# Performance work log

Hardware: AMD Instinct MI355X
Metric: run time of the kernel (lower is better)

The kernel has to match this reference:

```python
import jax, jax.numpy as jnp
import numpy as np

N = 50000          # nodes
E = 400000         # edges
MUL = 32           # multiplicity per irrep
NUM_NEIGHBORS = 8.0
INV_SQRT3 = 1.0 / np.sqrt(3.0)  # w3j(1,1,0) coefficient


def setup_inputs() -> dict:
    key = jax.random.key(0)
    ks = jax.random.split(key, 20)
    inp = {
        # node_input: 32x0e (dim 32) + 32x1o (dim 96) = 128
        "node_input": jax.random.normal(ks[0], (N, 4 * MUL), jnp.float32),
        "node_attr": jnp.ones((N, 1), jnp.float32),           # 1x0e trivial attr
        "edge_src": jax.random.randint(ks[1], (E,), 0, N, jnp.int32),
        "edge_dst": jax.random.randint(ks[2], (E,), 0, N, jnp.int32),
        "edge_attr": jax.random.normal(ks[3], (E, 4), jnp.float32),   # 1x0e + 1x1o
        "edge_scalars": jax.random.normal(ks[4], (E, 16), jnp.float32),
        # FullyConnectedTensorProduct weights (uvw, node_attr has mul 1)
        "w_sc0": jax.random.normal(ks[5], (MUL, MUL), jnp.float32),
        "w_sc1": jax.random.normal(ks[6], (MUL, MUL), jnp.float32),
        "w_lin1_0": jax.random.normal(ks[7], (MUL, MUL), jnp.float32),
        "w_lin1_1": jax.random.normal(ks[8], (MUL, MUL), jnp.float32),
        # radial FC net -> per-edge TP weights (numel = 4*MUL = 128)
        "fc_w1": jax.random.normal(ks[9], (16, 64), jnp.float32),
        "fc_w2": jax.random.normal(ks[10], (64, 4 * MUL), jnp.float32),
        # lin2: irreps_mid (64x0e+64x1o) x attr -> output
        "w_lin2_0": jax.random.normal(ks[11], (2 * MUL, MUL), jnp.float32),
        "w_lin2_1": jax.random.normal(ks[12], (2 * MUL, MUL), jnp.float32),
        # alpha: irreps_mid x attr -> 0e (zero-init in original; small randn for a nontrivial test)
        "w_alpha": 0.1 * jax.random.normal(ks[13], (2 * MUL, 1), jnp.float32),
        # sc_edges: irreps_mid x edge_attr -> edge_attr
        "w_se0a": jax.random.normal(ks[14], (2 * MUL,), jnp.float32),  # mid0e x ea0e -> 0e
        "w_se0b": jax.random.normal(ks[15], (2 * MUL,), jnp.float32),  # mid1o x ea1o -> 0e
        "w_se1a": jax.random.normal(ks[16], (2 * MUL,), jnp.float32),  # mid0e x ea1o -> 1o
        "w_se1b": jax.random.normal(ks[17], (2 * MUL,), jnp.float32),  # mid1o x ea0e -> 1o
    }
    return inp


def reference(node_input, node_attr, edge_src, edge_dst, edge_attr, edge_scalars,
              w_sc0, w_sc1, w_lin1_0, w_lin1_1, fc_w1, fc_w2,
              w_lin2_0, w_lin2_1, w_alpha, w_se0a, w_se0b, w_se1a, w_se1b):
    inv_nn = 1.0 / jnp.sqrt(jnp.asarray(NUM_NEIGHBORS, node_input.dtype))
    n = node_input.shape[0]
    x0 = node_input[:, :MUL]                       # (N, 32)   32x0e
    x1 = node_input[:, MUL:].reshape(n, MUL, 3)    # (N, 32, 3) 32x1o
    a = node_attr                                  # (N, 1)
    s_in = 1.0 / np.sqrt(MUL)                      # FCTP fan-in normalization

    # self-connection: FCTP(input, attr) -> output
    sc0 = (x0 @ w_sc0) * a * s_in
    sc1 = jnp.einsum('num,uw->nwm', x1, w_sc1) * a[:, :, None] * s_in
    node_self = jnp.concatenate([sc0, sc1.reshape(n, 3 * MUL)], axis=1)  # (N, 128)

    # lin1: FCTP(input, attr) -> input irreps
    f0 = (x0 @ w_lin1_0) * a * s_in
    f1 = jnp.einsum('num,uw->nwm', x1, w_lin1_1) * a[:, :, None] * s_in

    # gather source node features per edge
    g0 = f0[edge_src]                              # (E, 32)
    g1 = f1[edge_src]                              # (E, 32, 3)
    ea0 = edge_attr[:, :1]                         # (E, 1)   1x0e
    ea1 = edge_attr[:, 1:]                         # (E, 3)   1x1o

    # radial net -> per-edge TP weights (FullyConnectedNet with sin activation)
    h = jnp.sin(edge_scalars @ fc_w1 * (1.0 / np.sqrt(16.0)))
    w = h @ fc_w2 * (1.0 / np.sqrt(64.0))          # (E, 128)
    wA, wB, wC, wD = jnp.split(w, 4, axis=1)       # each (E, 32)

    # uvu tensor product, 4 instructions
    mA = wA * g0 * ea0                                           # 0e x 0e -> 0e
    mD = wD * jnp.einsum('eum,em->eu', g1, ea1) * INV_SQRT3      # 1o x 1o -> 0e
    mB = (wB * g0)[:, :, None] * ea1[:, None, :]                 # 0e x 1o -> 1o
    mC = (wC[:, :, None] * g1) * ea0[:, :, None]                 # 1o x 0e -> 1o
    mid0 = jnp.concatenate([mA, mD], axis=1)       # (E, 64)  64x0e
    mid1 = jnp.concatenate([mB, mC], axis=1)       # (E, 64, 3) 64x1o

    # scatter-add to destination nodes
    n0 = jax.ops.segment_sum(mid0, edge_dst, num_segments=n) * inv_nn
    n1 = jax.ops.segment_sum(mid1, edge_dst, num_segments=n) * inv_nn

    s_mid = 1.0 / np.sqrt(2 * MUL)
    out0 = (n0 @ w_lin2_0) * a * s_mid
    out1 = jnp.einsum('num,uw->nwm', n1, w_lin2_1) * a[:, :, None] * s_mid
    node_conv = jnp.concatenate([out0, out1.reshape(n, 3 * MUL)], axis=1)

    # alpha gate (sc.output_mask is all ones here, so alpha = 1 - 1 + alpha*1)
    alpha = (n0 @ w_alpha) * a * s_mid             # (N, 1)
    node_conv_out = node_self + alpha * node_conv  # (N, 128)

    # sc_edges: FCTP(mid, edge_attr) -> edge_attr irreps; fan-in = 128 per output
    s_se = 1.0 / np.sqrt(4 * MUL)
    se0 = ((mid0 @ w_se0a) * ea0[:, 0]
           + jnp.einsum('eum,em,u->e', mid1, ea1, w_se0b) * INV_SQRT3) * s_se
    se1 = ((mid0 @ w_se1a)[:, None] * ea1
           + jnp.einsum('eum,u->em', mid1, w_se1b) * ea0) * s_se
    edge_conv_out = edge_attr + jnp.concatenate([se0[:, None], se1], axis=1) * inv_nn

    return node_conv_out, edge_conv_out
```

## Files before the change

### kernel.cpp

```cpp
#include <hip/hip_runtime.h>
#include <math.h>

#define N_NODES 50000
#define E_EDGES 400000
#define NPRE_BLOCKS 6250
#define NHIST_BLOCKS 1563

typedef _Float16 f16x2 __attribute__((ext_vector_type(2)));
typedef _Float16 f16x4 __attribute__((ext_vector_type(4)));
typedef _Float16 f16x8 __attribute__((ext_vector_type(8)));
typedef float    f32x4 __attribute__((ext_vector_type(4)));

static constexpr float S_IN      = 0.17677669529663687f;
static constexpr float S_MID     = 0.125f;
static constexpr float S_SE      = 0.08838834764831843f;
static constexpr float INV_NN    = 0.35355339059327373f;
static constexpr float INV_SQRT3 = 0.5773502691896258f;
static constexpr float FC1_S     = 0.25f;
static constexpr float FC2_S     = 0.125f;

__device__ inline float wave_reduce_dpp(float v) {
    int x;
    x = __builtin_amdgcn_update_dpp(0, __float_as_int(v), 0x111, 0xf, 0xf, true); v += __int_as_float(x);
    x = __builtin_amdgcn_update_dpp(0, __float_as_int(v), 0x112, 0xf, 0xf, true); v += __int_as_float(x);
    x = __builtin_amdgcn_update_dpp(0, __float_as_int(v), 0x114, 0xf, 0xf, true); v += __int_as_float(x);
    x = __builtin_amdgcn_update_dpp(0, __float_as_int(v), 0x118, 0xf, 0xf, true); v += __int_as_float(x);
    x = __builtin_amdgcn_update_dpp(0, __float_as_int(v), 0x142, 0xa, 0xf, true); v += __int_as_float(x);
    x = __builtin_amdgcn_update_dpp(0, __float_as_int(v), 0x143, 0xc, 0xf, true); v += __int_as_float(x);
    return __int_as_float(__builtin_amdgcn_readlane(__float_as_int(v), 63));
}

__global__ __launch_bounds__(256) void pre_hist_kernel(
    const float* __restrict__ node_input, const float* __restrict__ node_attr,
    const float* __restrict__ w_sc0, const float* __restrict__ w_sc1,
    const float* __restrict__ w_lin1_0, const float* __restrict__ w_lin1_1,
    float* __restrict__ out_self, float* __restrict__ ws_f,
    const int* __restrict__ edge_dst, int* __restrict__ counts)
{
    const int t = threadIdx.x;
    if (blockIdx.x >= NPRE_BLOCKS) {
        const int e = (blockIdx.x - NPRE_BLOCKS) * 256 + t;
        if (e < E_EDGES) atomicAdd(&counts[edge_dst[e]], 1);
        return;
    }
    const int n0 = blockIdx.x * 8;
    __shared__ __align__(16) float sx[8 * 128];
    __shared__ float sa[8];
    ((float4*)sx)[t] = ((const float4*)(node_input + (size_t)n0 * 128))[t];
    if (t < 8) sa[t] = node_attr[n0 + t];
    __syncthreads();

    const int half = t >> 7;
    const int idx  = t & 127;
    float wcol[32];
    int m = 0;
    if (idx < 32) {
        const float* __restrict__ W = half ? w_lin1_0 : w_sc0;
        #pragma unroll
        for (int u = 0; u < 32; ++u) wcol[u] = W[u * 32 + idx];
    } else {
        const float* __restrict__ W = half ? w_lin1_1 : w_sc1;
        const int j = idx - 32;
        const int w = j / 3; m = j % 3;
        #pragma unroll
        for (int u = 0; u < 32; ++u) wcol[u] = W[u * 32 + w];
    }
    float* __restrict__ dstp = half ? ws_f : out_self;
    #pragma unroll
    for (int k = 0; k < 8; ++k) {
        const float* x = sx + k * 128;
        float acc = 0.f;
        if (idx < 32) {
            #pragma unroll
            for (int u = 0; u < 32; ++u) acc += x[u] * wcol[u];
        } else {
            #pragma unroll
            for (int u = 0; u < 32; ++u) acc += x[32 + u * 3 + m] * wcol[u];
        }
        dstp[(size_t)(n0 + k) * 128 + idx] = acc * sa[k] * S_IN;
    }
}

__global__ __launch_bounds__(1024) void scan_block_kernel(
    const int* __restrict__ counts, int* __restrict__ cursor, int* __restrict__ bsum)
{
    __shared__ int sd[1024];
    const int t   = threadIdx.x;
    const int idx = blockIdx.x * 1024 + t;
    const int c   = (idx < N_NODES) ? counts[idx] : 0;
    sd[t] = c;
    __syncthreads();
    for (int off = 1; off < 1024; off <<= 1) {
        const int v = (t >= off) ? sd[t - off] : 0;
        __syncthreads();
        sd[t] += v;
        __syncthreads();
    }
    if (idx < N_NODES) cursor[idx] = sd[t] - c;
    if (t == 1023) bsum[blockIdx.x] = sd[1023];
}

__global__ __launch_bounds__(1024) void scan_fixup_kernel(
    int* __restrict__ cursor, const int* __restrict__ bsum)
{
    __shared__ int boff_s;
    const int t = threadIdx.x;
    if (t < 64) {
        int v = (t < (int)blockIdx.x) ? bsum[t] : 0;
        #pragma unroll
        for (int off = 32; off >= 1; off >>= 1) v += __shfl_down(v, off, 64);
        if (t == 0) boff_s = v;
    }
    __syncthreads();
    const int idx = blockIdx.x * 1024 + t;
    if (idx < N_NODES) cursor[idx] += boff_s;
}

__global__ __launch_bounds__(256) void scatter_kernel(
    const int* __restrict__ edge_dst, int* __restrict__ cursor,
    int* __restrict__ sorted_eid)
{
    const int e = blockIdx.x * 256 + threadIdx.x;
    if (e < E_EDGES) {
        const int p = atomicAdd(&cursor[edge_dst[e]], 1);
        sorted_eid[p] = e;
    }
}

__global__ __launch_bounds__(256, 4) void edge_kernel(
    const float* __restrict__ ws_f,
    const int* __restrict__ edge_src, const int* __restrict__ edge_dst,
    const float* __restrict__ edge_attr, const float* __restrict__ edge_scalars,
    const float* __restrict__ fc_w1, const float* __restrict__ fc_w2,
    const float* __restrict__ w_se0a, const float* __restrict__ w_se0b,
    const float* __restrict__ w_se1a, const float* __restrict__ w_se1b,
    const int* __restrict__ sorted_eid,
    float* __restrict__ nacc, float* __restrict__ edge_out)
{
    __shared__ __align__(16) _Float16 sArena[18944];
    __shared__ __align__(16) float sEA[64 * 4];
    __shared__ __align__(16) float sDep[4][36];
    __shared__ int sSRC[64];
    __shared__ int sDST[64];
    __shared__ int sEID[64];

    _Float16* __restrict__ sW2T  = sArena;
    _Float16* __restrict__ sHT   = sArena + 9216;
    _Float16* __restrict__ sES   = sArena + 13824;
    _Float16* __restrict__ sW1T  = sArena + 16384;
    _Float16* __restrict__ sWt   = sArena;
    _Float16* __restrict__ sMidA = sArena + 8704;
    _Float16* __restrict__ sBT   = sArena + 12928;

    const int t    = threadIdx.x;
    const int lane = t & 63;
    const int wv   = t >> 6;
    const int quad = lane >> 4;
    const int mm   = lane & 15;
    const int e0   = blockIdx.x * 64;

    {
        const int k = t >> 4, n4 = (t & 15) * 4;
        float4 v = ((const float4*)fc_w1)[t];
        sW1T[(n4 + 0) * 40 + k] = (_Float16)v.x;
        sW1T[(n4 + 1) * 40 + k] = (_Float16)v.y;
        sW1T[(n4 + 2) * 40 + k] = (_Float16)v.z;
        sW1T[(n4 + 3) * 40 + k] = (_Float16)v.w;
        const f16x4 z4 = {(_Float16)0.f, (_Float16)0.f, (_Float16)0.f, (_Float16)0.f};
        *(f16x4*)&sW1T[(t >> 2) * 40 + 16 + (t & 3) * 4] = z4;
    }
    #pragma unroll
    for (int i = 0; i < 8; ++i) {
        const int u = t + i * 256;
        const int k = u >> 5, c4 = (u & 31) * 4;
        float4 v = ((const float4*)fc_w2)[u];
        sW2T[(c4 + 0) * 72 + k] = (_Float16)v.x;
        sW2T[(c4 + 1) * 72 + k] = (_Float16)v.y;
        sW2T[(c4 + 2) * 72 + k] = (_Float16)v.z;
        sW2T[(c4 + 3) * 72 + k] = (_Float16)v.w;
    }
    {
        const int e = t >> 2, k4 = (t & 3) * 4;
        const int eid = sorted_eid[e0 + e];
        float4 v = ((const float4*)edge_scalars)[(size_t)eid * 4 + (t & 3)];
        f16x4 p = {(_Float16)v.x, (_Float16)v.y, (_Float16)v.z, (_Float16)v.w};
        *(f16x4*)&sES[e * 40 + k4] = p;
        const f16x4 z4 = {(_Float16)0.f, (_Float16)0.f, (_Float16)0.f, (_Float16)0.f};
        *(f16x4*)&sES[e * 40 + 16 + k4] = z4;
    }
    if (t < 64) {
        const int eid = sorted_eid[e0 + t];
        *(float4*)&sEA[t * 4] = ((const float4*)edge_attr)[eid];
        sEID[t] = eid;
    } else if (t < 128) {
        sSRC[t - 64] = edge_src[sorted_eid[e0 + (t - 64)]];
    } else if (t < 192) {
        sDST[t - 128] = edge_dst[sorted_eid[e0 + (t - 128)]];
    }
    __syncthreads();

    const int eb = wv * 16;

    {
        const f16x8 b_es = *(const f16x8*)&sES[(eb + mm) * 40 + quad * 8];
        #pragma unroll
        for (int jt = 0; jt < 4; ++jt) {
            const f16x8 a_w1 = *(const f16x8*)&sW1T[(jt * 16 + mm) * 40 + quad * 8];
            f32x4 d = {0.f, 0.f, 0.f, 0.f};
            d = __builtin_amdgcn_mfma_f32_16x16x32_f16(a_w1, b_es, d, 0, 0, 0);
            f16x4 hv;
            hv[0] = (_Float16)__sinf(d[0] * FC1_S);
            hv[1] = (_Float16)__sinf(d[1] * FC1_S);
            hv[2] = (_Float16)__sinf(d[2] * FC1_S);
            hv[3] = (_Float16)__sinf(d[3] * FC1_S);
            *(f16x4*)&sHT[(eb + mm) * 72 + jt * 16 + quad * 4] = hv;
        }
    }
    __syncthreads();

    f32x4 dacc[8];
    {
        const f16x8 b_lo = *(const f16x8*)&sHT[(eb + mm) * 72 + quad * 8];
        const f16x8 b_hi = *(const f16x8*)&sHT[(eb + mm) * 72 + 32 + quad * 8];
        #pragma unroll
        for (int ct = 0; ct < 8; ++ct) {
            const f16x8 a_lo = *(const f16x8*)&sW2T[(ct * 16 + mm) * 72 + quad * 8];
            const f16x8 a_hi = *(const f16x8*)&sW2T[(ct * 16 + mm) * 72 + 32 + quad * 8];
            f32x4 d = {0.f, 0.f, 0.f, 0.f};
            d = __builtin_amdgcn_mfma_f32_16x16x32_f16(a_lo, b_lo, d, 0, 0, 0);
            d = __builtin_amdgcn_mfma_f32_16x16x32_f16(a_hi, b_hi, d, 0, 0, 0);
            dacc[ct] = d;
        }
    }
    __syncthreads();

    {
        #pragma unroll
        for (int ct = 0; ct < 8; ++ct) {
            f16x4 v;
            v[0] = (_Float16)(dacc[ct][0] * FC2_S);
            v[1] = (_Float16)(dacc[ct][1] * FC2_S);
            v[2] = (_Float16)(dacc[ct][2] * FC2_S);
            v[3] = (_Float16)(dacc[ct][3] * FC2_S);
            *(f16x4*)&sWt[(eb + mm) * 136 + ct * 16 + quad * 4] = v;
        }
        const f16x8 z8 = {};
        for (int i = t; i < 528; i += 256) *(f16x8*)&sBT[i * 8] = z8;
    }
    __syncthreads();
    {
        const int u = t & 63, p = t >> 6;
        const float ev = (p == 0) ? w_se0a[u] : w_se1b[u];
        const float ov = (p == 0) ? w_se1a[u] : w_se0b[u];
        sBT[(2 * p) * 264 + 4 * u + p]     = (_Float16)ev;
        sBT[(2 * p + 1) * 264 + 4 * u + p] = (_Float16)ov;
    }
    __syncthreads();

    const bool hi = lane >= 32;
    const int  u  = lane - 32;
    const int idxA = hi ? (32 + 3 * u) : lane;
    const int idxB = hi ? (33 + 3 * u) : lane;
    const int idxC = hi ? (34 + 3 * u) : lane;
    const int col1 = hi ? (96 + u) : lane;
    const int col2 = hi ? (64 + u) : (32 + lane);

    int   cur = -1;
    float am0 = 0.f, axx = 0.f, ayy = 0.f, azz = 0.f;
    _Float16* __restrict__ myA = sMidA + wv * 1056;
    const _Float16* __restrict__ arow = myA + (mm & 3) * 264;
    const _Float16* __restrict__ brow = sBT + mm * 264;

    for (int b = 0; b < 4; ++b) {
        float ga[4], gb[4], gc[4];
        #pragma unroll
        for (int i = 0; i < 4; ++i) {
            const int el = eb + b * 4 + i;
            const float* fr = ws_f + (size_t)sSRC[el] * 128;
            ga[i] = fr[idxA]; gb[i] = fr[idxB]; gc[i] = fr[idxC];
        }
        #pragma unroll
        for (int i = 0; i < 4; ++i) {
            const int el  = eb + b * 4 + i;
            const int dst = sDST[el];
            const float ea0 = sEA[el * 4 + 0];
            const float e1x = sEA[el * 4 + 1];
            const float e1y = sEA[el * 4 + 2];
            const float e1z = sEA[el * 4 + 3];
            const float w1v = (float)sWt[el * 136 + col1];
            const float w2v = (float)sWt[el * 136 + col2];

            float mid0, m1x, m1y, m1z;
            if (!hi) {
                mid0 = w1v * ga[i] * ea0;
                const float wbg = w2v * ga[i];
                m1x = wbg * e1x; m1y = wbg * e1y; m1z = wbg * e1z;
            } else {
                const float dot = ga[i] * e1x + gb[i] * e1y + gc[i] * e1z;
                mid0 = w1v * dot * INV_SQRT3;
                const float wce = w2v * ea0;
                m1x = wce * ga[i]; m1y = wce * gb[i]; m1z = wce * gc[i];
            }

            if (dst != cur) {
                if (cur >= 0) {
                    float* np_ = nacc + (size_t)cur * 256;
                    atomicAdd(np_ + lane, am0);
                    atomicAdd(np_ + 64 + lane * 3 + 0, axx);
                    atomicAdd(np_ + 64 + lane * 3 + 1, ayy);
                    atomicAdd(np_ + 64 + lane * 3 + 2, azz);
                }
                cur = dst; am0 = axx = ayy = azz = 0.f;
            }
            am0 += mid0; axx += m1x; ayy += m1y; azz += m1z;

            f16x4 mv;
            mv[0] = (_Float16)mid0; mv[1] = (_Float16)m1x;
            mv[2] = (_Float16)m1y;  mv[3] = (_Float16)m1z;
            *(f16x4*)&myA[i * 264 + 4 * lane] = mv;
        }

        f32x4 d = {0.f, 0.f, 0.f, 0.f};
        #pragma unroll
        for (int ks = 0; ks < 8; ++ks) {
            const f16x8 a  = *(const f16x8*)&arow[ks * 32 + quad * 8];
            const f16x8 bb = *(const f16x8*)&brow[ks * 32 + quad * 8];
            d = __builtin_amdgcn_mfma_f32_16x16x32_f16(a, bb, d, 0, 0, 0);
        }
        if (lane < 8) {
            float4 f4; f4.x = d[0]; f4.y = d[1]; f4.z = d[2]; f4.w = d[3];
            *(float4*)&sDep[wv][lane * 4] = f4;
        }
        if (lane < 4) {
            const int el = eb + b * 4 + lane;
            const float c0 = sDep[wv][ 0 + lane], c1 = sDep[wv][ 4 + lane];
            const float c2 = sDep[wv][ 8 + lane], c3 = sDep[wv][12 + lane];
            const float c4 = sDep[wv][16 + lane], c5 = sDep[wv][20 + lane];
            const float c6 = sDep[wv][24 + lane], c7 = sDep[wv][28 + lane];
            const float ea0 = sEA[el * 4 + 0];
            const float e1x = sEA[el * 4 + 1];
            const float e1y = sEA[el * 4 + 2];
            const float e1z = sEA[el * 4 + 3];
            const float s0 = c0 * ea0 + (c3 * e1x + c5 * e1y + c7 * e1z) * INV_SQRT3;
            float4 o;
            o.x = ea0 + s0 * S_SE * INV_NN;
            o.y = e1x + (c1 * e1x + c2 * ea0) * S_SE * INV_NN;
            o.z = e1y + (c1 * e1y + c4 * ea0) * S_SE * INV_NN;
            o.w = e1z + (c1 * e1z + c6 * ea0) * S_SE * INV_NN;
            *(float4*)&edge_out[(size_t)sEID[el] * 4] = o;
        }
    }
    if (cur >= 0) {
        float* np_ = nacc + (size_t)cur * 256;
        atomicAdd(np_ + lane, am0);
        atomicAdd(np_ + 64 + lane * 3 + 0, axx);
        atomicAdd(np_ + 64 + lane * 3 + 1, ayy);
        atomicAdd(np_ + 64 + lane * 3 + 2, azz);
    }
}

__global__ __launch_bounds__(128) void node_post_kernel(
    const float* __restrict__ nacc, const float* __restrict__ node_attr,
    const float* __restrict__ w_lin2_0, const float* __restrict__ w_lin2_1,
    const float* __restrict__ w_alpha, float* __restrict__ out)
{
    const int n0 = blockIdx.x * 8, t = threadIdx.x;
    __shared__ __align__(16) float sn[8 * 256];
    __shared__ float salpha[8];
    const float4* src = (const float4*)(nacc + (size_t)n0 * 256);
    #pragma unroll
    for (int i = 0; i < 4; ++i) ((float4*)sn)[t + i * 128] = src[t + i * 128];
    __syncthreads();

    if (t < 64) {
        const float wa = w_alpha[t];
        #pragma unroll
        for (int k = 0; k < 8; ++k) {
            const float r = wave_reduce_dpp(sn[k * 256 + t] * wa);
            if (t == 0) salpha[k] = r;
        }
    }
    __syncthreads();

    float wcol[64];
    int m = 0;
    if (t < 32) {
        #pragma unroll
        for (int u = 0; u < 64; ++u) wcol[u] = w_lin2_0[u * 32 + t];
    } else {
        const int j = t - 32; const int w = j / 3; m = j % 3;
        #pragma unroll
        for (int u = 0; u < 64; ++u) wcol[u] = w_lin2_1[u * 32 + w];
    }
    #pragma unroll
    for (int k = 0; k < 8; ++k) {
        const float* s = sn + k * 256;
        float acc = 0.f;
        if (t < 32) {
            #pragma unroll
            for (int u = 0; u < 64; ++u) acc += s[u] * wcol[u];
        } else {
            #pragma unroll
            for (int u = 0; u < 64; ++u) acc += s[64 + u * 3 + m] * wcol[u];
        }
        const float a  = node_attr[n0 + k];
        const float sc = a * S_MID * INV_NN;
        const size_t o = (size_t)(n0 + k) * 128 + t;
        out[o] = out[o] + (salpha[k] * sc) * (acc * sc);
    }
}

extern "C" void kernel_launch(void* const* d_in, const int* in_sizes, int n_in,
                              void* d_out, int out_size, void* d_ws, size_t ws_size,
                              hipStream_t stream)
{
    const float* node_input   = (const float*)d_in[0];
    const float* node_attr    = (const float*)d_in[1];
    const int*   edge_src     = (const int*)d_in[2];
    const int*   edge_dst     = (const int*)d_in[3];
    const float* edge_attr    = (const float*)d_in[4];
    const float* edge_scalars = (const float*)d_in[5];
    const float* w_sc0        = (const float*)d_in[6];
    const float* w_sc1        = (const float*)d_in[7];
    const float* w_lin1_0     = (const float*)d_in[8];
    const float* w_lin1_1     = (const float*)d_in[9];
    const float* fc_w1        = (const float*)d_in[10];
    const float* fc_w2        = (const float*)d_in[11];
    const float* w_lin2_0     = (const float*)d_in[12];
    const float* w_lin2_1     = (const float*)d_in[13];
    const float* w_alpha      = (const float*)d_in[14];
    const float* w_se0a       = (const float*)d_in[15];
    const float* w_se0b       = (const float*)d_in[16];
    const float* w_se1a       = (const float*)d_in[17];
    const float* w_se1b       = (const float*)d_in[18];

    float* out      = (float*)d_out;
    float* edge_out = out + (size_t)N_NODES * 128;

    float* ws_f   = (float*)d_ws;
    float* nacc   = ws_f + (size_t)N_NODES * 128;
    int*   counts = (int*)(nacc + (size_t)N_NODES * 256);
    int*   cursor = counts + N_NODES;
    int*   sid    = cursor + N_NODES;
    int*   bsum   = sid + E_EDGES;

    hipMemsetAsync(nacc, 0,
        ((size_t)N_NODES * 256 + N_NODES) * sizeof(float), stream);

    pre_hist_kernel<<<NPRE_BLOCKS + NHIST_BLOCKS, 256, 0, stream>>>(
        node_input, node_attr, w_sc0, w_sc1, w_lin1_0, w_lin1_1, out, ws_f,
        edge_dst, counts);

    scan_block_kernel<<<49, 1024, 0, stream>>>(counts, cursor, bsum);
    scan_fixup_kernel<<<49, 1024, 0, stream>>>(cursor, bsum);
    scatter_kernel<<<(E_EDGES + 255) / 256, 256, 0, stream>>>(edge_dst, cursor, sid);

    edge_kernel<<<E_EDGES / 64, 256, 0, stream>>>(
        ws_f, edge_src, edge_dst, edge_attr, edge_scalars, fc_w1, fc_w2,
        w_se0a, w_se0b, w_se1a, w_se1b, sid, nacc, edge_out);

    node_post_kernel<<<N_NODES / 8, 128, 0, stream>>>(
        nacc, node_attr, w_lin2_0, w_lin2_1, w_alpha, out);
}
```

Baseline: 413.1 us.

## Pretransform fp16 weights once and prefetch all gathers in edge kernel

An extra block in the pre kernel converts and transposes fc_w1, fc_w2 and the sc_edges weights into fp16 layouts in a workspace buffer. The edge kernel then copies them into LDS with vectorized loads instead of doing per-block scalar transposes and an extra barrier. It also hoists all 16 source-node gathers per wave ahead of the loop, pads the mid-A rows to 272 to ease bank conflicts, and splits the MFMA chain into two accumulators for ILP. The cost is more registers (48 gathered floats), which may lower occupancy.

```diff
diff --git a/kernel.cpp b/kernel.cpp
--- a/kernel.cpp
+++ b/kernel.cpp
@@ -18,6 +18,11 @@
 static constexpr float INV_SQRT3 = 0.5773502691896258f;
 static constexpr float FC1_S     = 0.25f;
 static constexpr float FC2_S     = 0.125f;
+
+#define WSW_W2T 0
+#define WSW_W1T 9216
+#define WSW_BT  11776
+#define WSW_TOTAL 16000
 
 __device__ inline float wave_reduce_dpp(float v) {
     int x;
@@ -34,10 +39,35 @@
     const float* __restrict__ node_input, const float* __restrict__ node_attr,
     const float* __restrict__ w_sc0, const float* __restrict__ w_sc1,
     const float* __restrict__ w_lin1_0, const float* __restrict__ w_lin1_1,
+    const float* __restrict__ fc_w1, const float* __restrict__ fc_w2,
+    const float* __restrict__ w_se0a, const float* __restrict__ w_se0b,
+    const float* __restrict__ w_se1a, const float* __restrict__ w_se1b,
     float* __restrict__ out_self, float* __restrict__ ws_f,
-    const int* __restrict__ edge_dst, int* __restrict__ counts)
+    const int* __restrict__ edge_dst, int* __restrict__ counts,
+    _Float16* __restrict__ wsW)
 {
     const int t = threadIdx.x;
+    if (blockIdx.x == NPRE_BLOCKS + NHIST_BLOCKS) {
+        for (int i = t; i < 8192; i += 256) {
+            const int c = i >> 6, k = i & 63;
+            wsW[WSW_W2T + c * 72 + k] = (_Float16)fc_w2[k * 128 + c];
+        }
+        for (int i = t; i < 2560; i += 256) {
+            const int j = i / 40, k = i - j * 40;
+            wsW[WSW_W1T + i] = (k < 16) ? (_Float16)fc_w1[k * 64 + j]
+                                        : (_Float16)0.f;
+        }
+        for (int i = t; i < 4224; i += 256) wsW[WSW_BT + i] = (_Float16)0.f;
+        __syncthreads();
+        {
+            const int u = t & 63, p = t >> 6;
+            const float ev = (p == 0) ? w_se0a[u] : w_se1b[u];
+            const float ov = (p == 0) ? w_se1a[u] : w_se0b[u];
+            wsW[WSW_BT + (2 * p) * 264 + 4 * u + p]     = (_Float16)ev;
+            wsW[WSW_BT + (2 * p + 1) * 264 + 4 * u + p] = (_Float16)ov;
+        }
+        return;
+    }
     if (blockIdx.x >= NPRE_BLOCKS) {
         const int e = (blockIdx.x - NPRE_BLOCKS) * 256 + t;
         if (e < E_EDGES) atomicAdd(&counts[edge_dst[e]], 1);
@@ -131,9 +161,7 @@
     const float* __restrict__ ws_f,
     const int* __restrict__ edge_src, const int* __restrict__ edge_dst,
     const float* __restrict__ edge_attr, const float* __restrict__ edge_scalars,
-    const float* __restrict__ fc_w1, const float* __restrict__ fc_w2,
-    const float* __restrict__ w_se0a, const float* __restrict__ w_se0b,
-    const float* __restrict__ w_se1a, const float* __restrict__ w_se1b,
+    const _Float16* __restrict__ wsW,
     const int* __restrict__ sorted_eid,
     float* __restrict__ nacc, float* __restrict__ edge_out)
 {
@@ -150,7 +178,7 @@
     _Float16* __restrict__ sW1T  = sArena + 16384;
     _Float16* __restrict__ sWt   = sArena;
     _Float16* __restrict__ sMidA = sArena + 8704;
-    _Float16* __restrict__ sBT   = sArena + 12928;
+    _Float16* __restrict__ sBT   = sArena + 13056;
 
     const int t    = threadIdx.x;
     const int lane = t & 63;
@@ -160,24 +188,17 @@
     const int e0   = blockIdx.x * 64;
 
     {
-        const int k = t >> 4, n4 = (t & 15) * 4;
-        float4 v = ((const float4*)fc_w1)[t];
-        sW1T[(n4 + 0) * 40 + k] = (_Float16)v.x;
-        sW1T[(n4 + 1) * 40 + k] = (_Float16)v.y;
-        sW1T[(n4 + 2) * 40 + k] = (_Float16)v.z;
-        sW1T[(n4 + 3) * 40 + k] = (_Float16)v.w;
-        const f16x4 z4 = {(_Float16)0.f, (_Float16)0.f, (_Float16)0.f, (_Float16)0.f};
-        *(f16x4*)&sW1T[(t >> 2) * 40 + 16 + (t & 3) * 4] = z4;
-    }
-    #pragma unroll
-    for (int i = 0; i < 8; ++i) {
-        const int u = t + i * 256;
-        const int k = u >> 5, c4 = (u & 31) * 4;
-        float4 v = ((const float4*)fc_w2)[u];
-        sW2T[(c4 + 0) * 72 + k] = (_Float16)v.x;
-        sW2T[(c4 + 1) * 72 + k] = (_Float16)v.y;
-        sW2T[(c4 + 2) * 72 + k] = (_Float16)v.z;
-        sW2T[(c4 + 3) * 72 + k] = (_Float16)v.w;
+        const f16x8* __restrict__ gW = (const f16x8*)wsW;
+        #pragma unroll
+        for (int i = 0; i < 5; ++i) {
+            const int idx = t + i * 256;
+            if (idx < 1152) ((f16x8*)sArena)[idx] = gW[idx];
+        }
+        #pragma unroll
+        for (int i = 0; i < 2; ++i) {
+            const int idx = t + i * 256;
+            if (idx < 320) *(f16x8*)&sArena[16384 + idx * 8] = gW[1152 + idx];
+        }
     }
     {
         const int e = t >> 2, k4 = (t & 3) * 4;
@@ -244,16 +265,12 @@
             v[3] = (_Float16)(dacc[ct][3] * FC2_S);
             *(f16x4*)&sWt[(eb + mm) * 136 + ct * 16 + quad * 4] = v;
         }
-        const f16x8 z8 = {};
-        for (int i = t; i < 528; i += 256) *(f16x8*)&sBT[i * 8] = z8;
-    }
-    __syncthreads();
-    {
-        const int u = t & 63, p = t >> 6;
-        const float ev = (p == 0) ? w_se0a[u] : w_se1b[u];
-        const float ov = (p == 0) ? w_se1a[u] : w_se0b[u];
-        sBT[(2 * p) * 264 + 4 * u + p]     = (_Float16)ev;
-        sBT[(2 * p + 1) * 264 + 4 * u + p] = (_Float16)ov;
+        const _Float16* __restrict__ gBT = wsW + WSW_BT;
+        #pragma unroll
+        for (int i = 0; i < 3; ++i) {
+            const int idx = t + i * 256;
+            if (idx < 528) *(f16x8*)&sBT[idx * 8] = *(const f16x8*)&gBT[idx * 8];
+        }
     }
     __syncthreads();
 
@@ -265,23 +282,24 @@
     const int col1 = hi ? (96 + u) : lane;
     const int col2 = hi ? (64 + u) : (32 + lane);
 
+    float ga[16], gb[16], gc[16];
+    #pragma unroll
+    for (int i = 0; i < 16; ++i) {
+        const float* fr = ws_f + (size_t)sSRC[eb + i] * 128;
+        ga[i] = fr[idxA]; gb[i] = fr[idxB]; gc[i] = fr[idxC];
+    }
+
     int   cur = -1;
     float am0 = 0.f, axx = 0.f, ayy = 0.f, azz = 0.f;
-    _Float16* __restrict__ myA = sMidA + wv * 1056;
-    const _Float16* __restrict__ arow = myA + (mm & 3) * 264;
+    _Float16* __restrict__ myA = sMidA + wv * 1088;
+    const _Float16* __restrict__ arow = myA + (mm & 3) * 272;
     const _Float16* __restrict__ brow = sBT + mm * 264;
 
     for (int b = 0; b < 4; ++b) {
-        float ga[4], gb[4], gc[4];
         #pragma unroll
         for (int i = 0; i < 4; ++i) {
-            const int el = eb + b * 4 + i;
-            const float* fr = ws_f + (size_t)sSRC[el] * 128;
-            ga[i] = fr[idxA]; gb[i] = fr[idxB]; gc[i] = fr[idxC];
-        }
-        #pragma unroll
-        for (int i = 0; i < 4; ++i) {
-            const int el  = eb + b * 4 + i;
+            const int e4  = b * 4 + i;
+            const int el  = eb + e4;
             const int dst = sDST[el];
             const float ea0 = sEA[el * 4 + 0];
             const float e1x = sEA[el * 4 + 1];
@@ -292,14 +310,14 @@
 
             float mid0, m1x, m1y, m1z;
             if (!hi) {
-                mid0 = w1v * ga[i] * ea0;
-                const float wbg = w2v * ga[i];
+                mid0 = w1v * ga[e4] * ea0;
+                const float wbg = w2v * ga[e4];
                 m1x = wbg * e1x; m1y = wbg * e1y; m1z = wbg * e1z;
             } else {
-                const float dot = ga[i] * e1x + gb[i] * e1y + gc[i] * e1z;
+                const float dot = ga[e4] * e1x + gb[e4] * e1y + gc[e4] * e1z;
                 mid0 = w1v * dot * INV_SQRT3;
                 const float wce = w2v * ea0;
-                m1x = wce * ga[i]; m1y = wce * gb[i]; m1z = wce * gc[i];
+                m1x = wce * ga[e4]; m1y = wce * gb[e4]; m1z = wce * gc[e4];
             }
 
             if (dst != cur) {
@@ -317,16 +335,24 @@
             f16x4 mv;
             mv[0] = (_Float16)mid0; mv[1] = (_Float16)m1x;
             mv[2] = (_Float16)m1y;  mv[3] = (_Float16)m1z;
-            *(f16x4*)&myA[i * 264 + 4 * lane] = mv;
-        }
-
-        f32x4 d = {0.f, 0.f, 0.f, 0.f};
-        #pragma unroll
-        for (int ks = 0; ks < 8; ++ks) {
-            const f16x8 a  = *(const f16x8*)&arow[ks * 32 + quad * 8];
-            const f16x8 bb = *(const f16x8*)&brow[ks * 32 + quad * 8];
-            d = __builtin_amdgcn_mfma_f32_16x16x32_f16(a, bb, d, 0, 0, 0);
-        }
+            *(f16x4*)&myA[i * 272 + 4 * lane] = mv;
+        }
+
+        f32x4 d0 = {0.f, 0.f, 0.f, 0.f};
+        f32x4 d1 = {0.f, 0.f, 0.f, 0.f};
+        #pragma unroll
+        for (int ks = 0; ks < 4; ++ks) {
+            const f16x8 a0  = *(const f16x8*)&arow[(2 * ks) * 32 + quad * 8];
+            const f16x8 bb0 = *(const f16x8*)&brow[(2 * ks) * 32 + quad * 8];
+            const f16x8 a1  = *(const f16x8*)&arow[(2 * ks + 1) * 32 + quad * 8];
+            const f16x8 bb1 = *(const f16x8*)&brow[(2 * ks + 1) * 32 + quad * 8];
+            d0 = __builtin_amdgcn_mfma_f32_16x16x32_f16(a0, bb0, d0, 0, 0, 0);
+            d1 = __builtin_amdgcn_mfma_f32_16x16x32_f16(a1, bb1, d1, 0, 0, 0);
+        }
+        f32x4 d;
+        d[0] = d0[0] + d1[0]; d[1] = d0[1] + d1[1];
+        d[2] = d0[2] + d1[2]; d[3] = d0[3] + d1[3];
+
         if (lane < 8) {
             float4 f4; f4.x = d[0]; f4.y = d[1]; f4.z = d[2]; f4.w = d[3];
             *(float4*)&sDep[wv][lane * 4] = f4;
@@ -443,21 +469,24 @@
     int*   cursor = counts + N_NODES;
     int*   sid    = cursor + N_NODES;
     int*   bsum   = sid + E_EDGES;
+    uintptr_t wp  = ((uintptr_t)(bsum + 64) + 15) & ~(uintptr_t)15;
+    _Float16* wsW = (_Float16*)wp;
 
     hipMemsetAsync(nacc, 0,
         ((size_t)N_NODES * 256 + N_NODES) * sizeof(float), stream);
 
-    pre_hist_kernel<<<NPRE_BLOCKS + NHIST_BLOCKS, 256, 0, stream>>>(
-        node_input, node_attr, w_sc0, w_sc1, w_lin1_0, w_lin1_1, out, ws_f,
-        edge_dst, counts);
+    pre_hist_kernel<<<NPRE_BLOCKS + NHIST_BLOCKS + 1, 256, 0, stream>>>(
+        node_input, node_attr, w_sc0, w_sc1, w_lin1_0, w_lin1_1,
+        fc_w1, fc_w2, w_se0a, w_se0b, w_se1a, w_se1b,
+        out, ws_f, edge_dst, counts, wsW);
 
     scan_block_kernel<<<49, 1024, 0, stream>>>(counts, cursor, bsum);
     scan_fixup_kernel<<<49, 1024, 0, stream>>>(cursor, bsum);
     scatter_kernel<<<(E_EDGES + 255) / 256, 256, 0, stream>>>(edge_dst, cursor, sid);
 
     edge_kernel<<<E_EDGES / 64, 256, 0, stream>>>(
-        ws_f, edge_src, edge_dst, edge_attr, edge_scalars, fc_w1, fc_w2,
-        w_se0a, w_se0b, w_se1a, w_se1b, sid, nacc, edge_out);
+        ws_f, edge_src, edge_dst, edge_attr, edge_scalars, wsW,
+        sid, nacc, edge_out);
 
     node_post_kernel<<<N_NODES / 8, 128, 0, stream>>>(
         nacc, node_attr, w_lin2_0, w_lin2_1, w_alpha, out);
```

After: 425.3 us. 1.03x slower.
